# Performance work log

Hardware: AMD Instinct MI355X
Metric: run time of the kernel (lower is better)

Reference implementation:

```python
import jax, jax.numpy as jnp
import numpy as np
import math

NUM_HEADS = 8

def setup_inputs() -> dict:
    key = jax.random.key(0)
    ks = jax.random.split(key, 20)
    N, n, M, E = 4096, 3, 16, 256
    nE = 65536
    s = lambda k, shape: (jax.random.normal(k, shape, jnp.float32) * 0.02)
    return {
        "equ": jax.random.normal(ks[0], (N, n, M), jnp.float32),
        "h": jax.random.normal(ks[1], (N, E), jnp.float32),
        "edge_index": jax.random.randint(ks[2], (2, nE), 0, N),
        "edge_fea": jax.random.normal(ks[3], (nE, 4), jnp.float32),
        "W_equ": s(ks[4], (M, E)),
        "W_gproj": s(ks[5], (E, 32)),
        "W_vg": s(ks[6], (E, E)),
        "W_g1": s(ks[7], (32 * 32, 2 * E)), "b_g1": jnp.zeros((2 * E,), jnp.float32),
        "W_g2": s(ks[8], (2 * E, E)), "b_g2": jnp.zeros((E,), jnp.float32),
        "W_q": s(ks[9], (2 * E, E)), "b_q": jnp.zeros((E,), jnp.float32),
        "W_k": s(ks[10], (2 * E, E)), "b_k": jnp.zeros((E,), jnp.float32),
        "W_v": s(ks[11], (2 * E, E)), "b_v": jnp.zeros((E,), jnp.float32),
        "W_ng": s(ks[12], (E, E)), "b_ng": jnp.zeros((E,), jnp.float32),
        "W_gout": s(ks[13], (E, E)),
        "W_gdec": s(ks[14], (E, M)),
        "W_hdec": s(ks[15], (E, E)), "b_hdec": jnp.zeros((E,), jnp.float32),
    }


def reference(equ, h, edge_index, edge_fea, W_equ, W_gproj, W_vg, W_g1, b_g1,
              W_g2, b_g2, W_q, b_q, W_k, b_k, W_v, b_v, W_ng, b_ng,
              W_gout, W_gdec, W_hdec, b_hdec):
    # edge_index / edge_fea are unused in the original forward (dead args).
    N, n, M = equ.shape
    E = W_equ.shape[1]
    H = NUM_HEADS
    D = E // H
    scaling = D ** -0.5
    sqrtE = math.sqrt(E)

    g_src = (equ @ W_equ) * sqrtE                     # [N, n, E]
    h_src = h * sqrtE                                 # [N, E]

    g2 = g_src @ W_gproj                              # [N, n, 32]
    gram = jnp.einsum('nia,nib->nab', g2, g2)         # [N, 32, 32]
    g2 = gram.reshape(N, 32 * 32)
    g2 = jax.nn.relu(g2 @ W_g1 + b_g1) @ W_g2 + b_g2  # [N, E]

    h2 = jnp.concatenate([g2, h_src], axis=-1)        # [N, 2E]
    q = ((h2 @ W_q + b_q) * scaling).reshape(N, H, D)
    k = (h2 @ W_k + b_k).reshape(N, H, D)
    v = (h2 @ W_v + b_v).reshape(N, H, D)
    vg = (g_src @ W_vg).reshape(N, n, H, D)           # [N, n, H, D]

    attn = jax.nn.softmax(jnp.einsum('nhd,mhd->hnm', q, k), axis=-1)  # [H, N, N]

    out_v = jnp.einsum('hnm,mhd->nhd', attn, v).reshape(N, E)
    h_src1 = out_v @ W_ng + b_ng                      # [N, E]

    # Same attention probs reused for the vector channel (torch does repeat+bmm;
    # we broadcast instead of materializing the repeated [n*H, N, N] tensor).
    out_g = jnp.einsum('hnm,mvhd->nvhd', attn, vg).reshape(N, n, E)
    g_src1 = out_g @ W_gout                           # [N, n, E]

    g_src = g_src + g_src1
    h_src = h_src + h_src1
    equ_out = g_src @ W_gdec                          # [N, n, M]
    h_out = h_src @ W_hdec + b_hdec                   # [N, E]
    return (equ_out, h_out)
```

## Files before the change

### kernel.cpp

```cpp
#include <hip/hip_runtime.h>
#include <hip/hip_bf16.h>

typedef __attribute__((ext_vector_type(8))) short short8;
typedef __attribute__((ext_vector_type(4))) short bhalf4;
typedef __attribute__((ext_vector_type(4))) float floatx4;

constexpr int N_ = 4096;
constexpr float SQRT_E = 16.0f;
constexpr float QSCALE = 0.17677669529663687f * 1.4426950408889634f;

__device__ __forceinline__ ushort f2bf(float x) {
  __hip_bfloat16 h = __float2bfloat16(x);
  return *reinterpret_cast<ushort*>(&h);
}
__device__ __forceinline__ float bf2f(ushort b) {
  unsigned int u = ((unsigned int)b) << 16;
  return __uint_as_float(u);
}

__device__ __forceinline__ void do_transpose(
    const float* __restrict__ src, ushort* __restrict__ dsth,
    ushort* __restrict__ dstl, int R, int C, int lb, int cb_shift,
    float* smem, int hasLo)
{
  float (*tile)[33] = (float(*)[33])smem;
  const int r0 = (lb >> cb_shift) * 32;
  const int c0 = (lb & ((1 << cb_shift) - 1)) * 32;
  const int tx = threadIdx.x & 31, ty = threadIdx.x >> 5;
  #pragma unroll
  for (int p = 0; p < 4; ++p) {
    const int lr = p*8 + ty;
    tile[lr][tx] = (r0+lr < R && c0+tx < C) ? src[(size_t)(r0+lr)*C + c0 + tx] : 0.f;
  }
  __syncthreads();
  #pragma unroll
  for (int p = 0; p < 4; ++p) {
    const int dc = p*8 + ty;
    if (c0+dc < C && r0+tx < R) {
      const float v = tile[tx][dc];
      const ushort hi = f2bf(v);
      dsth[(size_t)(c0+dc)*R + r0 + tx] = hi;
      if (hasLo) dstl[(size_t)(c0+dc)*R + r0 + tx] = f2bf(v - bf2f(hi));
    }
  }
}

__global__ __launch_bounds__(256) void k_prep(
    const float* __restrict__ equ, const float* __restrict__ h,
    const float* __restrict__ W_equ, const float* __restrict__ W_gproj,
    const float* __restrict__ W_g1, const float* __restrict__ W_g2,
    const float* __restrict__ W_q, const float* __restrict__ W_k,
    const float* __restrict__ W_v, const float* __restrict__ W_vg,
    const float* __restrict__ W_ng, const float* __restrict__ W_gout,
    const float* __restrict__ W_hdec, const float* __restrict__ W_gdec,
    ushort* __restrict__ Wg1t, ushort* __restrict__ Wg2t,
    ushort* __restrict__ Wth, ushort* __restrict__ Wtl,
    ushort* __restrict__ Wvgt, ushort* __restrict__ Wngt,
    ushort* __restrict__ Wgoutt, ushort* __restrict__ Whdect,
    ushort* __restrict__ Wgdect,
    ushort* __restrict__ h2h, ushort* __restrict__ h2l,
    ushort* __restrict__ g_src_b, ushort* __restrict__ gram_b,
    float* __restrict__ pre0)
{
  __shared__ __align__(16) float smem[1120];
  const int b = blockIdx.x;
  const int t = threadIdx.x;

  if (b < 512) {
    do_transpose(W_g1, Wg1t, nullptr, 1024, 512, b, 4, smem, 0);
  } else if (b < 640) {
    do_transpose(W_g2, Wg2t, nullptr, 512, 256, b-512, 3, smem, 0);
  } else if (b < 768) {
    do_transpose(W_q, Wth, Wtl, 512, 256, b-640, 3, smem, 1);
  } else if (b < 896) {
    do_transpose(W_k, Wth + 256*512, Wtl + 256*512, 512, 256, b-768, 3, smem, 1);
  } else if (b < 1024) {
    do_transpose(W_v, Wth + 512*512, Wtl + 512*512, 512, 256, b-896, 3, smem, 1);
  } else if (b < 1088) {
    do_transpose(W_vg, Wvgt, nullptr, 256, 256, b-1024, 3, smem, 0);
  } else if (b < 1152) {
    do_transpose(W_ng, Wngt, nullptr, 256, 256, b-1088, 3, smem, 0);
  } else if (b < 1216) {
    do_transpose(W_gout, Wgoutt, nullptr, 256, 256, b-1152, 3, smem, 0);
  } else if (b < 1280) {
    do_transpose(W_hdec, Whdect, nullptr, 256, 256, b-1216, 3, smem, 0);
  } else if (b < 1288) {
    do_transpose(W_gdec, Wgdect, nullptr, 256, 16, b-1280, 0, smem, 0);
  } else if (b < 5384) {
    const int i = b - 1288;
    const float v = h[(size_t)i*256 + t] * SQRT_E;
    const ushort hi = f2bf(v);
    h2h[(size_t)i*512 + 256 + t] = hi;
    h2l[(size_t)i*512 + 256 + t] = f2bf(v - bf2f(hi));
  } else {
    float* eq   = smem;
    float* gs   = smem + 48;
    float* g2p  = smem + 816;
    float* part = smem + 912;
    const int i = b - 5384;
    if (t < 48) eq[t] = equ[(size_t)i*48 + t];
    __syncthreads();
    #pragma unroll
    for (int j = 0; j < 3; ++j) {
      float s = 0.f;
      #pragma unroll
      for (int m = 0; m < 16; ++m) s += eq[j*16+m] * W_equ[m*256 + t];
      s *= SQRT_E;
      gs[j*256 + t] = s;
      g_src_b[((size_t)i*3 + j)*256 + t] = f2bf(s);
    }
    __syncthreads();
    if (t < 192) {
      const int o = t % 96, half = t / 96;
      const int j = o >> 5, a = o & 31;
      const int e0 = half * 128;
      float s = 0.f;
      for (int e = 0; e < 128; ++e)
        s += gs[j*256 + e0 + e] * W_gproj[(size_t)(e0+e)*32 + a];
      part[t] = s;
    }
    __syncthreads();
    if (t < 96) g2p[t] = part[t] + part[96 + t];
    __syncthreads();
    #pragma unroll
    for (int r = 0; r < 4; ++r) {
      const int idx = r*256 + t;
      const int a = idx >> 5, bb = idx & 31;
      const float s = g2p[a]*g2p[bb] + g2p[32+a]*g2p[32+bb] + g2p[64+a]*g2p[64+bb];
      gram_b[(size_t)i*1024 + idx] = f2bf(s);
    }
    if (t < 192) {
      const int j = t >> 6, ks = (t >> 4) & 3, mc = t & 15;
      const int e0 = ks * 64;
      float s = 0.f;
      for (int e = 0; e < 64; ++e)
        s += gs[j*256 + e0 + e] * W_gdec[(size_t)(e0 + e)*16 + mc];
      part[t] = s;
    }
    __syncthreads();
    if (t < 48) {
      const int j = t >> 4, mc = t & 15;
      pre0[((size_t)i*3 + j)*16 + mc] =
          part[j*64 + mc] + part[j*64 + 16 + mc] +
          part[j*64 + 32 + mc] + part[j*64 + 48 + mc];
    }
  }
}

template<int KTOT>
__device__ __forceinline__ void gemm_core(
    const ushort* __restrict__ A, const ushort* __restrict__ Bt,
    int bM, int bN, floatx4 acc[4], ushort* As, ushort* Bs)
{
  const int t = threadIdx.x;
  const int wave = t >> 6, lane = t & 63, quad = lane >> 4, m = lane & 15;
  #pragma unroll
  for (int ct = 0; ct < 4; ++ct) acc[ct] = {0.f, 0.f, 0.f, 0.f};
  const int ca = t*2, cb = t*2 + 1;
  const int ra = ca >> 3, pa = ca & 7;
  const int rb = cb >> 3, pb = cb & 7;
  const ushort* pA0 = A  + (size_t)(bM+ra)*KTOT + pa*8;
  const ushort* pA1 = A  + (size_t)(bM+rb)*KTOT + pb*8;
  const ushort* pB0 = Bt + (size_t)(bN+ra)*KTOT + pa*8;
  const ushort* pB1 = Bt + (size_t)(bN+rb)*KTOT + pb*8;
  short8 rA0 = *(const short8*)pA0, rA1 = *(const short8*)pA1;
  short8 rB0 = *(const short8*)pB0, rB1 = *(const short8*)pB1;
  for (int k0 = 0; k0 < KTOT; k0 += 64) {
    __syncthreads();
    *(short8*)&As[ra*72 + pa*8] = rA0;
    *(short8*)&As[rb*72 + pb*8] = rA1;
    *(short8*)&Bs[ra*72 + pa*8] = rB0;
    *(short8*)&Bs[rb*72 + pb*8] = rB1;
    if (k0 + 64 < KTOT) {
      pA0 += 64; pA1 += 64; pB0 += 64; pB1 += 64;
      rA0 = *(const short8*)pA0; rA1 = *(const short8*)pA1;
      rB0 = *(const short8*)pB0; rB1 = *(const short8*)pB1;
    }
    __syncthreads();
    #pragma unroll
    for (int ks = 0; ks < 2; ++ks) {
      const short8 af = *(const short8*)&As[(wave*16 + m)*72 + ks*32 + quad*8];
      #pragma unroll
      for (int ct = 0; ct < 4; ++ct) {
        const short8 bf = *(const short8*)&Bs[(ct*16 + m)*72 + ks*32 + quad*8];
        acc[ct] = __builtin_amdgcn_mfma_f32_16x16x32_bf16(af, bf, acc[ct], 0, 0, 0);
      }
    }
  }
}

template<int KTOT>
__device__ __forceinline__ void gemm_core3(
    const ushort* __restrict__ Ah, const ushort* __restrict__ Al,
    const ushort* __restrict__ Bth, const ushort* __restrict__ Btl,
    int bM, int bN, floatx4 acc[4],
    ushort* Ash, ushort* Asl, ushort* Bsh, ushort* Bsl)
{
  const int t = threadIdx.x;
  const int wave = t >> 6, lane = t & 63, quad = lane >> 4, m = lane & 15;
  #pragma unroll
  for (int ct = 0; ct < 4; ++ct) acc[ct] = {0.f, 0.f, 0.f, 0.f};
  const int ca = t*2, cb = t*2 + 1;
  const int ra = ca >> 3, pa = ca & 7;
  const int rb = cb >> 3, pb = cb & 7;
  const ushort* pAh0 = Ah  + (size_t)(bM+ra)*KTOT + pa*8;
  const ushort* pAh1 = Ah  + (size_t)(bM+rb)*KTOT + pb*8;
  const ushort* pAl0 = Al  + (size_t)(bM+ra)*KTOT + pa*8;
  const ushort* pAl1 = Al  + (size_t)(bM+rb)*KTOT + pb*8;
  const ushort* pBh0 = Bth + (size_t)(bN+ra)*KTOT + pa*8;
  const ushort* pBh1 = Bth + (size_t)(bN+rb)*KTOT + pb*8;
  const ushort* pBl0 = Btl + (size_t)(bN+ra)*KTOT + pa*8;
  const ushort* pBl1 = Btl + (size_t)(bN+rb)*KTOT + pb*8;
  short8 rAh0 = *(const short8*)pAh0, rAh1 = *(const short8*)pAh1;
  short8 rAl0 = *(const short8*)pAl0, rAl1 = *(const short8*)pAl1;
  short8 rBh0 = *(const short8*)pBh0, rBh1 = *(const short8*)pBh1;
  short8 rBl0 = *(const short8*)pBl0, rBl1 = *(const short8*)pBl1;
  for (int k0 = 0; k0 < KTOT; k0 += 64) {
    __syncthreads();
    *(short8*)&Ash[ra*72 + pa*8] = rAh0;
    *(short8*)&Ash[rb*72 + pb*8] = rAh1;
    *(short8*)&Asl[ra*72 + pa*8] = rAl0;
    *(short8*)&Asl[rb*72 + pb*8] = rAl1;
    *(short8*)&Bsh[ra*72 + pa*8] = rBh0;
    *(short8*)&Bsh[rb*72 + pb*8] = rBh1;
    *(short8*)&Bsl[ra*72 + pa*8] = rBl0;
    *(short8*)&Bsl[rb*72 + pb*8] = rBl1;
    if (k0 + 64 < KTOT) {
      pAh0 += 64; pAh1 += 64; pAl0 += 64; pAl1 += 64;
      pBh0 += 64; pBh1 += 64; pBl0 += 64; pBl1 += 64;
      rAh0 = *(const short8*)pAh0; rAh1 = *(const short8*)pAh1;
      rAl0 = *(const short8*)pAl0; rAl1 = *(const short8*)pAl1;
      rBh0 = *(const short8*)pBh0; rBh1 = *(const short8*)pBh1;
      rBl0 = *(const short8*)pBl0; rBl1 = *(const short8*)pBl1;
    }
    __syncthreads();
    #pragma unroll
    for (int ks = 0; ks < 2; ++ks) {
      const short8 ah = *(const short8*)&Ash[(wave*16 + m)*72 + ks*32 + quad*8];
      const short8 al = *(const short8*)&Asl[(wave*16 + m)*72 + ks*32 + quad*8];
      #pragma unroll
      for (int ct = 0; ct < 4; ++ct) {
        const short8 bh = *(const short8*)&Bsh[(ct*16 + m)*72 + ks*32 + quad*8];
        const short8 bl = *(const short8*)&Bsl[(ct*16 + m)*72 + ks*32 + quad*8];
        acc[ct] = __builtin_amdgcn_mfma_f32_16x16x32_bf16(ah, bl, acc[ct], 0, 0, 0);
        acc[ct] = __builtin_amdgcn_mfma_f32_16x16x32_bf16(al, bh, acc[ct], 0, 0, 0);
        acc[ct] = __builtin_amdgcn_mfma_f32_16x16x32_bf16(ah, bh, acc[ct], 0, 0, 0);
      }
    }
  }
}

__global__ __launch_bounds__(256) void k_g1(
    const ushort* __restrict__ gram_b, const ushort* __restrict__ Wg1t,
    const float* __restrict__ b_g1, ushort* __restrict__ hidden)
{
  __shared__ __align__(16) ushort As[64*72], Bs[64*72];
  floatx4 acc[4];
  const int bM = blockIdx.x*64, bN = blockIdx.y*64;
  gemm_core<1024>(gram_b, Wg1t, bM, bN, acc, As, Bs);
  const int lane = threadIdx.x & 63, wave = threadIdx.x >> 6;
  const int quad = lane >> 4, m = lane & 15;
  #pragma unroll
  for (int ct = 0; ct < 4; ++ct) {
    const int c = bN + ct*16 + m;
    #pragma unroll
    for (int r = 0; r < 4; ++r) {
      const int i = bM + wave*16 + quad*4 + r;
      hidden[(size_t)i*512 + c] = f2bf(fmaxf(acc[ct][r] + b_g1[c], 0.f));
    }
  }
}

__global__ __launch_bounds__(256) void k_g2(
    const ushort* __restrict__ hidden, const ushort* __restrict__ Wg2t,
    const float* __restrict__ b_g2, ushort* __restrict__ h2h, ushort* __restrict__ h2l)
{
  __shared__ __align__(16) ushort As[64*72], Bs[64*72];
  floatx4 acc[4];
  const int bM = blockIdx.x*64, bN = blockIdx.y*64;
  gemm_core<512>(hidden, Wg2t, bM, bN, acc, As, Bs);
  const int lane = threadIdx.x & 63, wave = threadIdx.x >> 6;
  const int quad = lane >> 4, m = lane & 15;
  #pragma unroll
  for (int ct = 0; ct < 4; ++ct) {
    const int c = bN + ct*16 + m;
    #pragma unroll
    for (int r = 0; r < 4; ++r) {
      const int i = bM + wave*16 + quad*4 + r;
      const float s = acc[ct][r] + b_g2[c];
      const ushort hi = f2bf(s);
      h2h[(size_t)i*512 + c] = hi;
      h2l[(size_t)i*512 + c] = f2bf(s - bf2f(hi));
    }
  }
}

__global__ __launch_bounds__(256) void k_g34(
    const ushort* __restrict__ h2h, const ushort* __restrict__ h2l,
    const ushort* __restrict__ Wth, const ushort* __restrict__ Wtl,
    const float* __restrict__ b_q, const float* __restrict__ b_k,
    const float* __restrict__ b_v,
    const ushort* __restrict__ g_src_b, const ushort* __restrict__ Wvgt,
    float* __restrict__ q_ws, ushort* __restrict__ kh,
    ushort* __restrict__ vt)
{
  __shared__ __align__(16) ushort S0[64*72], S1[64*72], S2[64*72], S3[64*72];
  const int lb = blockIdx.y*192 + blockIdx.x;
  const int lane = threadIdx.x & 63, wave = threadIdx.x >> 6;
  const int quad = lane >> 4, m = lane & 15;
  floatx4 acc[4];
  if (lb < 768) {
    const int bM = (lb & 63)*64, bN = (lb >> 6)*64;
    if (bN < 512) {
      gemm_core3<512>(h2h, h2l, Wth, Wtl, bM, bN, acc, S0, S1, S2, S3);
      #pragma unroll
      for (int ct = 0; ct < 4; ++ct) {
        const int c = bN + ct*16 + m;
        #pragma unroll
        for (int r = 0; r < 4; ++r) {
          const int i = bM + wave*16 + quad*4 + r;
          if (c < 256) {
            const float s = acc[ct][r] + b_q[c];
            q_ws[((size_t)(c >> 5)*N_ + i)*32 + (c & 31)] = s * QSCALE;
          } else {
            const int cc = c - 256;
            const float s = acc[ct][r] + b_k[cc];
            kh[((size_t)(cc >> 5)*N_ + i)*32 + (cc & 31)] = f2bf(s);
          }
        }
      }
    } else {
      gemm_core<512>(h2h, Wth, bM, bN, acc, S0, S1);
      #pragma unroll
      for (int ct = 0; ct < 4; ++ct) {
        const int cc = bN + ct*16 + m - 512;
        #pragma unroll
        for (int r = 0; r < 4; ++r) {
          const int i = bM + wave*16 + quad*4 + r;
          const float s = acc[ct][r] + b_v[cc];
          vt[((size_t)(cc >> 5)*128 + (cc & 31))*N_ + i] = f2bf(s);
        }
      }
    }
  } else {
    const int lb2 = lb - 768;
    const int bM = (lb2 >> 2)*64, bN = (lb2 & 3)*64;
    gemm_core<256>(g_src_b, Wvgt, bM, bN, acc, S0, S1);
    #pragma unroll
    for (int ct = 0; ct < 4; ++ct) {
      const int c = bN + ct*16 + m;
      const int hh = c >> 5, d = c & 31;
      #pragma unroll
      for (int r = 0; r < 4; ++r) {
        const int i3 = bM + wave*16 + quad*4 + r;
        const int i = i3 / 3, j = i3 - 3*i;
        vt[((size_t)hh*128 + 32 + j*32 + d)*N_ + i] = f2bf(acc[ct][r]);
      }
    }
  }
}

__global__ __launch_bounds__(256, 8) void k3_attn(
    const float* __restrict__ q_ws, const ushort* __restrict__ kh,
    const ushort* __restrict__ vt,
    ushort* __restrict__ Po0, ushort* __restrict__ Po1,
    ushort* __restrict__ Po2, ushort* __restrict__ Po3,
    float* __restrict__ Pml)
{
  __shared__ __align__(16) ushort Khs[64*40];
  __shared__ __align__(16) ushort Vs[128*64];

  const int t    = threadIdx.x;
  const int wave = t >> 6;
  const int lane = t & 63;
  const int quad = lane >> 4;
  const int m    = lane & 15;
  const int h    = blockIdx.y;
  const int s    = blockIdx.z;
  const int n0q  = blockIdx.x * 64;

  const int ktb = s * 16;
  const int kte = ktb + 16;

  union { short8 v; ushort u[8]; } Aqh, Aql;
  {
    const float* qp = q_ws + ((size_t)h*N_ + n0q + wave*16 + m)*32 + quad*8;
    #pragma unroll
    for (int jj = 0; jj < 8; ++jj) {
      const float x = qp[jj];
      const ushort hi = f2bf(x);
      Aqh.u[jj] = hi;
      Aql.u[jj] = f2bf(x - bf2f(hi));
    }
  }

  union { short8 v; ushort u[8]; } onesf;
  {
    const ushort ov = (m == 0) ? (ushort)0x3F80 : (ushort)0;
    #pragma unroll
    for (int jj = 0; jj < 8; ++jj) onesf.u[jj] = ov;
  }

  floatx4 Of[8];
  #pragma unroll
  for (int nt = 0; nt < 8; ++nt) Of[nt] = {0.f, 0.f, 0.f, 0.f};
  floatx4 Of8 = {0.f, 0.f, 0.f, 0.f};
  float mi = -3.0e38f;

  const int krow = t >> 2, kch = (t & 3) * 8;
  const ushort* pKh = kh + ((size_t)h*N_ + ktb*64 + krow)*32 + kch;

  const ushort* pV[4];
  int wv0[4], wv1[4];
  #pragma unroll
  for (int p = 0; p < 4; ++p) {
    const int idx = p*256 + t, row = idx >> 3, g = idx & 7;
    pV[p] = vt + ((size_t)h*128 + row)*N_ + ktb*64 + g*8;
    const int sb0  = 32*(g>>2) + 16*(g&1) + 4*((g>>1)&1);
    const int blk0 = sb0 >> 3, off = sb0 & 4, r7 = row & 7;
    wv0[p] = row*64 + ((blk0       ^ r7) * 8) + off;
    wv1[p] = row*64 + (((blk0 + 1) ^ r7) * 8) + off;
  }

  short8 rK0 = *(const short8*)pKh;
  short8 rV[4];
  #pragma unroll
  for (int p = 0; p < 4; ++p) rV[p] = *(const short8*)pV[p];

  const int x7 = m & 7;

  for (int kt = ktb; kt < kte; ++kt) {
    __syncthreads();
    *(short8*)&Khs[krow*40 + kch] = rK0;
    #pragma unroll
    for (int p = 0; p < 4; ++p) {
      union { short8 v; bhalf4 h2[2]; } tmp;
      tmp.v = rV[p];
      *(bhalf4*)&Vs[wv0[p]] = tmp.h2[0];
      *(bhalf4*)&Vs[wv1[p]] = tmp.h2[1];
    }
    if (kt + 1 < kte) {
      pKh += 2048;
      rK0 = *(const short8*)pKh;
      #pragma unroll
      for (int p = 0; p < 4; ++p) { pV[p] += 64; rV[p] = *(const short8*)pV[p]; }
    }
    __syncthreads();

    floatx4 sf[4];
    #pragma unroll
    for (int kb = 0; kb < 4; ++kb) {
      const short8 bkh = *(const short8*)&Khs[(kb*16 + m)*40 + quad*8];
      floatx4 sv = {0.f, 0.f, 0.f, 0.f};
      sv = __builtin_amdgcn_mfma_f32_16x16x32_bf16(bkh, Aql.v, sv, 0, 0, 0);
      sv = __builtin_amdgcn_mfma_f32_16x16x32_bf16(bkh, Aqh.v, sv, 0, 0, 0);
      sf[kb] = sv;
    }

    float nm = fmaxf(fmaxf(sf[0][0], sf[0][1]), fmaxf(sf[0][2], sf[0][3]));
    nm = fmaxf(nm, fmaxf(fmaxf(sf[1][0], sf[1][1]), fmaxf(sf[1][2], sf[1][3])));
    nm = fmaxf(nm, fmaxf(fmaxf(sf[2][0], sf[2][1]), fmaxf(sf[2][2], sf[2][3])));
    nm = fmaxf(nm, fmaxf(fmaxf(sf[3][0], sf[3][1]), fmaxf(sf[3][2], sf[3][3])));
    nm = fmaxf(nm, __shfl_xor(nm, 16));
    nm = fmaxf(nm, __shfl_xor(nm, 32));

    if (__any(nm > mi + 20.f)) {
      const float mn = fmaxf(mi, nm);
      const float al = exp2f(mi - mn);
      mi = mn;
      #pragma unroll
      for (int nt = 0; nt < 8; ++nt) {
        Of[nt][0] *= al; Of[nt][1] *= al; Of[nt][2] *= al; Of[nt][3] *= al;
      }
      Of8[0] *= al; Of8[1] *= al; Of8[2] *= al; Of8[3] *= al;
    }

    const float base = 1064866805.0f - mi*8388608.0f;
    union { short8 v; unsigned int u[4]; } pk[2];
    #pragma unroll
    for (int kb = 0; kb < 4; ++kb) {
      int p0 = (int)(sf[kb][0]*8388608.0f + base); p0 = p0 < 0 ? 0 : p0;
      int p1 = (int)(sf[kb][1]*8388608.0f + base); p1 = p1 < 0 ? 0 : p1;
      int p2 = (int)(sf[kb][2]*8388608.0f + base); p2 = p2 < 0 ? 0 : p2;
      int p3 = (int)(sf[kb][3]*8388608.0f + base); p3 = p3 < 0 ? 0 : p3;
      pk[kb >> 1].u[(kb & 1)*2 + 0] = ((unsigned)p0 >> 16) | ((unsigned)p1 & 0xffff0000u);
      pk[kb >> 1].u[(kb & 1)*2 + 1] = ((unsigned)p2 >> 16) | ((unsigned)p3 & 0xffff0000u);
    }

    #pragma unroll
    for (int ks = 0; ks < 2; ++ks) {
      #pragma unroll
      for (int nt = 0; nt < 8; ++nt) {
        const short8 av = *(const short8*)&Vs[(nt*16 + m)*64 + (((ks*4 + quad) ^ x7) * 8)];
        Of[nt] = __builtin_amdgcn_mfma_f32_16x16x32_bf16(av, pk[ks].v, Of[nt], 0, 0, 0);
      }
      Of8 = __builtin_amdgcn_mfma_f32_16x16x32_bf16(onesf.v, pk[ks].v, Of8, 0, 0, 0);
    }
  }

  const float denom = __shfl(Of8[0], m);
  const float linv = 1.0f / denom;

  ushort* Po = (s == 0) ? Po0 : ((s == 1) ? Po1 : ((s == 2) ? Po2 : Po3));
  const int n = n0q + wave*16 + m;
  #pragma unroll
  for (int nt = 0; nt < 8; ++nt) {
    unsigned int lo = (unsigned)f2bf(Of[nt][0] * linv) | ((unsigned)f2bf(Of[nt][1] * linv) << 16);
    unsigned int hi = (unsigned)f2bf(Of[nt][2] * linv) | ((unsigned)f2bf(Of[nt][3] * linv) << 16);
    uint2 pkd; pkd.x = lo; pkd.y = hi;
    *(uint2*)&Po[((size_t)h*N_ + n)*128 + nt*16 + quad*4] = pkd;
  }
  if (quad == 0) {
    Pml[(((size_t)s*8 + h)*N_ + n)*2 + 0] = mi;
    Pml[(((size_t)s*8 + h)*N_ + n)*2 + 1] = Of8[0];
  }
}

__global__ __launch_bounds__(256) void k_merge(
    const ushort* __restrict__ Po0, const ushort* __restrict__ Po1,
    const ushort* __restrict__ Po2, const ushort* __restrict__ Po3,
    const float* __restrict__ Pml,
    ushort* __restrict__ out_v_b, ushort* __restrict__ out_g_b)
{
  const int idx = blockIdx.x*256 + threadIdx.x;
  const int c0 = (idx & 15) * 8;
  const int n  = (idx >> 4) & 4095;
  const int h  = idx >> 16;
  float mm[4], ll[4];
  #pragma unroll
  for (int s = 0; s < 4; ++s) {
    mm[s] = Pml[(((size_t)s*8 + h)*N_ + n)*2 + 0];
    ll[s] = Pml[(((size_t)s*8 + h)*N_ + n)*2 + 1];
  }
  const float M = fmaxf(fmaxf(mm[0], mm[1]), fmaxf(mm[2], mm[3]));
  float w[4], tot = 0.f;
  #pragma unroll
  for (int s = 0; s < 4; ++s) { w[s] = exp2f(mm[s] - M) * ll[s]; tot += w[s]; }
  const float inv = 1.0f / tot;
  union { short8 v; ushort u[8]; } a, b, c, d, res;
  a.v = *(const short8*)&Po0[((size_t)h*N_ + n)*128 + c0];
  b.v = *(const short8*)&Po1[((size_t)h*N_ + n)*128 + c0];
  c.v = *(const short8*)&Po2[((size_t)h*N_ + n)*128 + c0];
  d.v = *(const short8*)&Po3[((size_t)h*N_ + n)*128 + c0];
  #pragma unroll
  for (int j = 0; j < 8; ++j)
    res.u[j] = f2bf((w[0]*bf2f(a.u[j]) + w[1]*bf2f(b.u[j]) +
                     w[2]*bf2f(c.u[j]) + w[3]*bf2f(d.u[j])) * inv);
  if (c0 < 32) {
    *(short8*)&out_v_b[(size_t)n*256 + h*32 + c0] = res.v;
  } else {
    const int j = (c0 - 32) >> 5, cc = (c0 - 32) & 31;
    *(short8*)&out_g_b[((size_t)n*3 + j)*256 + h*32 + cc] = res.v;
  }
}

__global__ __launch_bounds__(256) void k56ab(
    const ushort* __restrict__ out_v_b, const ushort* __restrict__ Wngt,
    const float* __restrict__ b_ng, const float* __restrict__ h,
    ushort* __restrict__ tmp_b,
    const ushort* __restrict__ out_g_b, const ushort* __restrict__ Wgoutt,
    ushort* __restrict__ gsum_b)
{
  __shared__ __align__(16) ushort As[64*72], Bs[64*72];
  floatx4 acc[4];
  const int lane = threadIdx.x & 63, wave = threadIdx.x >> 6;
  const int quad = lane >> 4, m = lane & 15;
  const int bN = blockIdx.y*64;
  if (blockIdx.x < 64) {
    const int bM = blockIdx.x*64;
    gemm_core<256>(out_v_b, Wngt, bM, bN, acc, As, Bs);
    #pragma unroll
    for (int ct = 0; ct < 4; ++ct) {
      const int c = bN + ct*16 + m;
      #pragma unroll
      for (int r = 0; r < 4; ++r) {
        const int i = bM + wave*16 + quad*4 + r;
        tmp_b[(size_t)i*256 + c] =
            f2bf(acc[ct][r] + b_ng[c] + h[(size_t)i*256 + c] * SQRT_E);
      }
    }
  } else {
    const int bM = (blockIdx.x - 64)*64;
    gemm_core<256>(out_g_b, Wgoutt, bM, bN, acc, As, Bs);
    #pragma unroll
    for (int ct = 0; ct < 4; ++ct) {
      const int c = bN + ct*16 + m;
      #pragma unroll
      for (int r = 0; r < 4; ++r) {
        const int i = bM + wave*16 + quad*4 + r;
        gsum_b[(size_t)i*256 + c] = f2bf(acc[ct][r]);
      }
    }
  }
}

__global__ __launch_bounds__(256) void k56cd(
    const ushort* __restrict__ tmp_b, const ushort* __restrict__ Whdect,
    const float* __restrict__ b_hdec,
    const ushort* __restrict__ gsum_b, const ushort* __restrict__ Wgdect,
    const float* __restrict__ pre0,
    float* __restrict__ out)
{
  __shared__ __align__(16) ushort As[64*72], Bs[64*72];
  const int t = threadIdx.x;
  const int lane = t & 63, wave = t >> 6;
  const int quad = lane >> 4, m = lane & 15;
  if (blockIdx.x < 64) {
    floatx4 acc[4];
    const int bM = blockIdx.x*64, bN = blockIdx.y*64;
    gemm_core<256>(tmp_b, Whdect, bM, bN, acc, As, Bs);
    #pragma unroll
    for (int ct = 0; ct < 4; ++ct) {
      const int c = bN + ct*16 + m;
      #pragma unroll
      for (int r = 0; r < 4; ++r) {
        const int i = bM + wave*16 + quad*4 + r;
        out[196608 + (size_t)i*256 + c] = acc[ct][r] + b_hdec[c];
      }
    }
  } else if (blockIdx.y == 0) {
    const int bM = (blockIdx.x - 64)*64;
    floatx4 acc = {0.f, 0.f, 0.f, 0.f};
    const int row = t >> 2, kq = (t & 3) * 8;
    for (int k0 = 0; k0 < 256; k0 += 32) {
      __syncthreads();
      *(short8*)&As[row*40 + kq] = *(const short8*)&gsum_b[(size_t)(bM+row)*256 + k0 + kq];
      if (t < 64)
        *(short8*)&Bs[(t>>2)*40 + kq] = *(const short8*)&Wgdect[(size_t)(t>>2)*256 + k0 + kq];
      __syncthreads();
      const short8 af = *(const short8*)&As[(wave*16 + m)*40 + quad*8];
      const short8 bf = *(const short8*)&Bs[m*40 + quad*8];
      acc = __builtin_amdgcn_mfma_f32_16x16x32_bf16(af, bf, acc, 0, 0, 0);
    }
    #pragma unroll
    for (int r = 0; r < 4; ++r) {
      const int i3 = bM + wave*16 + quad*4 + r;
      out[(size_t)i3*16 + m] = acc[r] + pre0[(size_t)i3*16 + m];
    }
  }
}

extern "C" void kernel_launch(void* const* d_in, const int* in_sizes, int n_in,
                              void* d_out, int out_size, void* d_ws, size_t ws_size,
                              hipStream_t stream) {
  const float* equ    = (const float*)d_in[0];
  const float* h      = (const float*)d_in[1];
  const float* W_equ  = (const float*)d_in[4];
  const float* W_gproj= (const float*)d_in[5];
  const float* W_vg   = (const float*)d_in[6];
  const float* W_g1   = (const float*)d_in[7];
  const float* b_g1   = (const float*)d_in[8];
  const float* W_g2   = (const float*)d_in[9];
  const float* b_g2   = (const float*)d_in[10];
  const float* W_q    = (const float*)d_in[11];
  const float* b_q    = (const float*)d_in[12];
  const float* W_k    = (const float*)d_in[13];
  const float* b_k    = (const float*)d_in[14];
  const float* W_v    = (const float*)d_in[15];
  const float* b_v    = (const float*)d_in[16];
  const float* W_ng   = (const float*)d_in[17];
  const float* b_ng   = (const float*)d_in[18];
  const float* W_gout = (const float*)d_in[19];
  const float* W_gdec = (const float*)d_in[20];
  const float* W_hdec = (const float*)d_in[21];
  const float* b_hdec = (const float*)d_in[22];
  float* out = (float*)d_out;

  char* wsb = (char*)d_ws;
  constexpr size_t MiB = 1048576;
  float*  q_ws    = (float*) (wsb +  0*MiB);
  ushort* kh      = (ushort*)(wsb +  4*MiB);
  float*  Pml     = (float*) (wsb +  6*MiB);
  float*  pre0    = (float*) (wsb +  7*MiB);
  ushort* vt      = (ushort*)(wsb +  8*MiB);
  ushort* h2h     = (ushort*)(wsb + 17*MiB);
  ushort* h2l     = (ushort*)(wsb + 21*MiB);
  ushort* g_src_b = (ushort*)(wsb + 25*MiB);
  ushort* wbase   = (ushort*)(wsb + 31*MiB);
  ushort* Wg1t = wbase;
  ushort* Wg2t = wbase + 524288;
  ushort* Wth  = wbase + 655360;
  ushort* Wtl  = wbase + 1048576;
  ushort* Wvgt = wbase + 1441792;
  ushort* gram_b  = (ushort*)(wsb + 34*MiB);
  ushort* hidden  = (ushort*)(wsb + 42*MiB);
  ushort* Po0     = (ushort*)(wsb + 17*MiB);
  ushort* Po1     = (ushort*)(wsb + 25*MiB);
  ushort* Po2     = (ushort*)(wsb + 34*MiB);
  ushort* Po3     = (ushort*)(wsb + 42*MiB);
  ushort* wbase2  = (ushort*)(wsb + 50*MiB);
  ushort* Wngt   = wbase2;
  ushort* Wgoutt = wbase2 + 65536;
  ushort* Whdect = wbase2 + 131072;
  ushort* Wgdect = wbase2 + 196608;
  ushort* out_v_b = (ushort*)(wsb +  4*MiB);
  ushort* out_g_b = (ushort*)(wsb +  8*MiB);
  ushort* tmp_b   = (ushort*)(wsb + 17*MiB);
  ushort* gsum_b  = (ushort*)(wsb + 25*MiB);

  k_prep<<<9480, 256, 0, stream>>>(
      equ, h, W_equ, W_gproj, W_g1, W_g2, W_q, W_k, W_v,
      W_vg, W_ng, W_gout, W_hdec, W_gdec,
      Wg1t, Wg2t, Wth, Wtl, Wvgt, Wngt, Wgoutt, Whdect, Wgdect,
      h2h, h2l, g_src_b, gram_b, pre0);

  k_g1<<<dim3(64, 8), 256, 0, stream>>>(gram_b, Wg1t, b_g1, hidden);
  k_g2<<<dim3(64, 4), 256, 0, stream>>>(hidden, Wg2t, b_g2, h2h, h2l);
  k_g34<<<dim3(192, 8), 256, 0, stream>>>(h2h, h2l, Wth, Wtl, b_q, b_k, b_v,
                                          g_src_b, Wvgt, q_ws, kh, vt);

  dim3 g3(64, 8, 4);
  k3_attn<<<g3, 256, 0, stream>>>(q_ws, kh, vt, Po0, Po1, Po2, Po3, Pml);
  k_merge<<<2048, 256, 0, stream>>>(Po0, Po1, Po2, Po3, Pml, out_v_b, out_g_b);

  k56ab<<<dim3(256, 4), 256, 0, stream>>>(out_v_b, Wngt, b_ng, h, tmp_b,
                                          out_g_b, Wgoutt, gsum_b);
  k56cd<<<dim3(256, 4), 256, 0, stream>>>(tmp_b, Whdect, b_hdec,
                                          gsum_b, Wgdect, pre0, out);
}
```

Measured before the change: 279.9 us.

## Process two query tiles per wave in attention kernel to reuse K/V LDS tiles

Each wave of the split-K attention kernel now handles two 16-row query groups, so a block covers 128 queries and the grid is halved. Every K and V tile staged in LDS, and each V fragment read from LDS, feeds twice as many MFMAs, which halves global K/V traffic and LDS reads per query. The denominator is now passed through a small shared buffer instead of a shuffle. The cost is about twice the accumulator registers, with launch bounds lowered to 3 blocks, so occupancy drops and there are fewer blocks to hide latency.

```diff
diff --git a/kernel.cpp b/kernel.cpp
--- a/kernel.cpp
+++ b/kernel.cpp
@@ -360,7 +360,7 @@
   }
 }
 
-__global__ __launch_bounds__(256, 8) void k3_attn(
+__global__ __launch_bounds__(256, 3) void k3_attn(
     const float* __restrict__ q_ws, const ushort* __restrict__ kh,
     const ushort* __restrict__ vt,
     ushort* __restrict__ Po0, ushort* __restrict__ Po1,
@@ -369,6 +369,7 @@
 {
   __shared__ __align__(16) ushort Khs[64*40];
   __shared__ __align__(16) ushort Vs[128*64];
+  __shared__ float li_s[128];
 
   const int t    = threadIdx.x;
   const int wave = t >> 6;
@@ -377,20 +378,21 @@
   const int m    = lane & 15;
   const int h    = blockIdx.y;
   const int s    = blockIdx.z;
-  const int n0q  = blockIdx.x * 64;
+  const int n0q  = blockIdx.x * 128;
 
   const int ktb = s * 16;
   const int kte = ktb + 16;
 
-  union { short8 v; ushort u[8]; } Aqh, Aql;
-  {
-    const float* qp = q_ws + ((size_t)h*N_ + n0q + wave*16 + m)*32 + quad*8;
+  union { short8 v; ushort u[8]; } Aqh[2], Aql[2];
+  #pragma unroll
+  for (int g = 0; g < 2; ++g) {
+    const float* qp = q_ws + ((size_t)h*N_ + n0q + (wave*2+g)*16 + m)*32 + quad*8;
     #pragma unroll
     for (int jj = 0; jj < 8; ++jj) {
       const float x = qp[jj];
       const ushort hi = f2bf(x);
-      Aqh.u[jj] = hi;
-      Aql.u[jj] = f2bf(x - bf2f(hi));
+      Aqh[g].u[jj] = hi;
+      Aql[g].u[jj] = f2bf(x - bf2f(hi));
     }
   }
 
@@ -401,11 +403,15 @@
     for (int jj = 0; jj < 8; ++jj) onesf.u[jj] = ov;
   }
 
-  floatx4 Of[8];
-  #pragma unroll
-  for (int nt = 0; nt < 8; ++nt) Of[nt] = {0.f, 0.f, 0.f, 0.f};
-  floatx4 Of8 = {0.f, 0.f, 0.f, 0.f};
-  float mi = -3.0e38f;
+  floatx4 Of[2][8];
+  #pragma unroll
+  for (int g = 0; g < 2; ++g)
+    #pragma unroll
+    for (int nt = 0; nt < 8; ++nt) Of[g][nt] = {0.f, 0.f, 0.f, 0.f};
+  floatx4 Of8[2];
+  Of8[0] = {0.f, 0.f, 0.f, 0.f};
+  Of8[1] = {0.f, 0.f, 0.f, 0.f};
+  float mi[2] = {-3.0e38f, -3.0e38f};
 
   const int krow = t >> 2, kch = (t & 3) * 8;
   const ushort* pKh = kh + ((size_t)h*N_ + ktb*64 + krow)*32 + kch;
@@ -447,72 +453,89 @@
     }
     __syncthreads();
 
-    floatx4 sf[4];
-    #pragma unroll
-    for (int kb = 0; kb < 4; ++kb) {
-      const short8 bkh = *(const short8*)&Khs[(kb*16 + m)*40 + quad*8];
-      floatx4 sv = {0.f, 0.f, 0.f, 0.f};
-      sv = __builtin_amdgcn_mfma_f32_16x16x32_bf16(bkh, Aql.v, sv, 0, 0, 0);
-      sv = __builtin_amdgcn_mfma_f32_16x16x32_bf16(bkh, Aqh.v, sv, 0, 0, 0);
-      sf[kb] = sv;
-    }
-
-    float nm = fmaxf(fmaxf(sf[0][0], sf[0][1]), fmaxf(sf[0][2], sf[0][3]));
-    nm = fmaxf(nm, fmaxf(fmaxf(sf[1][0], sf[1][1]), fmaxf(sf[1][2], sf[1][3])));
-    nm = fmaxf(nm, fmaxf(fmaxf(sf[2][0], sf[2][1]), fmaxf(sf[2][2], sf[2][3])));
-    nm = fmaxf(nm, fmaxf(fmaxf(sf[3][0], sf[3][1]), fmaxf(sf[3][2], sf[3][3])));
-    nm = fmaxf(nm, __shfl_xor(nm, 16));
-    nm = fmaxf(nm, __shfl_xor(nm, 32));
-
-    if (__any(nm > mi + 20.f)) {
-      const float mn = fmaxf(mi, nm);
-      const float al = exp2f(mi - mn);
-      mi = mn;
-      #pragma unroll
-      for (int nt = 0; nt < 8; ++nt) {
-        Of[nt][0] *= al; Of[nt][1] *= al; Of[nt][2] *= al; Of[nt][3] *= al;
-      }
-      Of8[0] *= al; Of8[1] *= al; Of8[2] *= al; Of8[3] *= al;
-    }
-
-    const float base = 1064866805.0f - mi*8388608.0f;
-    union { short8 v; unsigned int u[4]; } pk[2];
-    #pragma unroll
-    for (int kb = 0; kb < 4; ++kb) {
-      int p0 = (int)(sf[kb][0]*8388608.0f + base); p0 = p0 < 0 ? 0 : p0;
-      int p1 = (int)(sf[kb][1]*8388608.0f + base); p1 = p1 < 0 ? 0 : p1;
-      int p2 = (int)(sf[kb][2]*8388608.0f + base); p2 = p2 < 0 ? 0 : p2;
-      int p3 = (int)(sf[kb][3]*8388608.0f + base); p3 = p3 < 0 ? 0 : p3;
-      pk[kb >> 1].u[(kb & 1)*2 + 0] = ((unsigned)p0 >> 16) | ((unsigned)p1 & 0xffff0000u);
-      pk[kb >> 1].u[(kb & 1)*2 + 1] = ((unsigned)p2 >> 16) | ((unsigned)p3 & 0xffff0000u);
-    }
-
-    #pragma unroll
-    for (int ks = 0; ks < 2; ++ks) {
-      #pragma unroll
-      for (int nt = 0; nt < 8; ++nt) {
-        const short8 av = *(const short8*)&Vs[(nt*16 + m)*64 + (((ks*4 + quad) ^ x7) * 8)];
-        Of[nt] = __builtin_amdgcn_mfma_f32_16x16x32_bf16(av, pk[ks].v, Of[nt], 0, 0, 0);
-      }
-      Of8 = __builtin_amdgcn_mfma_f32_16x16x32_bf16(onesf.v, pk[ks].v, Of8, 0, 0, 0);
-    }
-  }
-
-  const float denom = __shfl(Of8[0], m);
-  const float linv = 1.0f / denom;
+    union { short8 v; unsigned int u[4]; } pkA[2], pkB[2];
+    #pragma unroll
+    for (int g = 0; g < 2; ++g) {
+      floatx4 sf[4];
+      #pragma unroll
+      for (int kb = 0; kb < 4; ++kb) {
+        const short8 bkh = *(const short8*)&Khs[(kb*16 + m)*40 + quad*8];
+        floatx4 sv = {0.f, 0.f, 0.f, 0.f};
+        sv = __builtin_amdgcn_mfma_f32_16x16x32_bf16(bkh, Aql[g].v, sv, 0, 0, 0);
+        sv = __builtin_amdgcn_mfma_f32_16x16x32_bf16(bkh, Aqh[g].v, sv, 0, 0, 0);
+        sf[kb] = sv;
+      }
+
+      float nm = fmaxf(fmaxf(sf[0][0], sf[0][1]), fmaxf(sf[0][2], sf[0][3]));
+      nm = fmaxf(nm, fmaxf(fmaxf(sf[1][0], sf[1][1]), fmaxf(sf[1][2], sf[1][3])));
+      nm = fmaxf(nm, fmaxf(fmaxf(sf[2][0], sf[2][1]), fmaxf(sf[2][2], sf[2][3])));
+      nm = fmaxf(nm, fmaxf(fmaxf(sf[3][0], sf[3][1]), fmaxf(sf[3][2], sf[3][3])));
+      nm = fmaxf(nm, __shfl_xor(nm, 16));
+      nm = fmaxf(nm, __shfl_xor(nm, 32));
+
+      if (__any(nm > mi[g] + 20.f)) {
+        const float mn = fmaxf(mi[g], nm);
+        const float al = exp2f(mi[g] - mn);
+        mi[g] = mn;
+        #pragma unroll
+        for (int nt = 0; nt < 8; ++nt) {
+          Of[g][nt][0] *= al; Of[g][nt][1] *= al;
+          Of[g][nt][2] *= al; Of[g][nt][3] *= al;
+        }
+        Of8[g][0] *= al; Of8[g][1] *= al; Of8[g][2] *= al; Of8[g][3] *= al;
+      }
+
+      const float base = 1064866805.0f - mi[g]*8388608.0f;
+      #pragma unroll
+      for (int kb = 0; kb < 4; ++kb) {
+        int p0 = (int)(sf[kb][0]*8388608.0f + base); p0 = p0 < 0 ? 0 : p0;
+        int p1 = (int)(sf[kb][1]*8388608.0f + base); p1 = p1 < 0 ? 0 : p1;
+        int p2 = (int)(sf[kb][2]*8388608.0f + base); p2 = p2 < 0 ? 0 : p2;
+        int p3 = (int)(sf[kb][3]*8388608.0f + base); p3 = p3 < 0 ? 0 : p3;
+        const unsigned wlo = ((unsigned)p0 >> 16) | ((unsigned)p1 & 0xffff0000u);
+        const unsigned whi = ((unsigned)p2 >> 16) | ((unsigned)p3 & 0xffff0000u);
+        if (kb < 2) { pkA[g].u[kb*2] = wlo; pkA[g].u[kb*2+1] = whi; }
+        else        { pkB[g].u[(kb-2)*2] = wlo; pkB[g].u[(kb-2)*2+1] = whi; }
+      }
+    }
+
+    #pragma unroll
+    for (int nt = 0; nt < 8; ++nt) {
+      const short8 av0 = *(const short8*)&Vs[(nt*16 + m)*64 + ((quad ^ x7) * 8)];
+      Of[0][nt] = __builtin_amdgcn_mfma_f32_16x16x32_bf16(av0, pkA[0].v, Of[0][nt], 0, 0, 0);
+      Of[1][nt] = __builtin_amdgcn_mfma_f32_16x16x32_bf16(av0, pkA[1].v, Of[1][nt], 0, 0, 0);
+      const short8 av1 = *(const short8*)&Vs[(nt*16 + m)*64 + (((4 + quad) ^ x7) * 8)];
+      Of[0][nt] = __builtin_amdgcn_mfma_f32_16x16x32_bf16(av1, pkB[0].v, Of[0][nt], 0, 0, 0);
+      Of[1][nt] = __builtin_amdgcn_mfma_f32_16x16x32_bf16(av1, pkB[1].v, Of[1][nt], 0, 0, 0);
+    }
+    Of8[0] = __builtin_amdgcn_mfma_f32_16x16x32_bf16(onesf.v, pkA[0].v, Of8[0], 0, 0, 0);
+    Of8[1] = __builtin_amdgcn_mfma_f32_16x16x32_bf16(onesf.v, pkA[1].v, Of8[1], 0, 0, 0);
+    Of8[0] = __builtin_amdgcn_mfma_f32_16x16x32_bf16(onesf.v, pkB[0].v, Of8[0], 0, 0, 0);
+    Of8[1] = __builtin_amdgcn_mfma_f32_16x16x32_bf16(onesf.v, pkB[1].v, Of8[1], 0, 0, 0);
+  }
+
+  if (quad == 0) {
+    li_s[wave*32 + m]      = Of8[0][0];
+    li_s[wave*32 + 16 + m] = Of8[1][0];
+  }
+  __syncthreads();
 
   ushort* Po = (s == 0) ? Po0 : ((s == 1) ? Po1 : ((s == 2) ? Po2 : Po3));
-  const int n = n0q + wave*16 + m;
-  #pragma unroll
-  for (int nt = 0; nt < 8; ++nt) {
-    unsigned int lo = (unsigned)f2bf(Of[nt][0] * linv) | ((unsigned)f2bf(Of[nt][1] * linv) << 16);
-    unsigned int hi = (unsigned)f2bf(Of[nt][2] * linv) | ((unsigned)f2bf(Of[nt][3] * linv) << 16);
-    uint2 pkd; pkd.x = lo; pkd.y = hi;
-    *(uint2*)&Po[((size_t)h*N_ + n)*128 + nt*16 + quad*4] = pkd;
-  }
-  if (quad == 0) {
-    Pml[(((size_t)s*8 + h)*N_ + n)*2 + 0] = mi;
-    Pml[(((size_t)s*8 + h)*N_ + n)*2 + 1] = Of8[0];
+  #pragma unroll
+  for (int g = 0; g < 2; ++g) {
+    const float linv = 1.0f / li_s[wave*32 + g*16 + m];
+    const int n = n0q + (wave*2 + g)*16 + m;
+    #pragma unroll
+    for (int nt = 0; nt < 8; ++nt) {
+      unsigned int lo = (unsigned)f2bf(Of[g][nt][0] * linv) | ((unsigned)f2bf(Of[g][nt][1] * linv) << 16);
+      unsigned int hi = (unsigned)f2bf(Of[g][nt][2] * linv) | ((unsigned)f2bf(Of[g][nt][3] * linv) << 16);
+      uint2 pkd; pkd.x = lo; pkd.y = hi;
+      *(uint2*)&Po[((size_t)h*N_ + n)*128 + nt*16 + quad*4] = pkd;
+    }
+    if (quad == 0) {
+      Pml[(((size_t)s*8 + h)*N_ + n)*2 + 0] = mi[g];
+      Pml[(((size_t)s*8 + h)*N_ + n)*2 + 1] = Of8[g][0];
+    }
   }
 }
 
@@ -709,7 +732,7 @@
   k_g34<<<dim3(192, 8), 256, 0, stream>>>(h2h, h2l, Wth, Wtl, b_q, b_k, b_v,
                                           g_src_b, Wvgt, q_ws, kh, vt);
 
-  dim3 g3(64, 8, 4);
+  dim3 g3(32, 8, 4);
   k3_attn<<<g3, 256, 0, stream>>>(q_ws, kh, vt, Po0, Po1, Po2, Po3, Pml);
   k_merge<<<2048, 256, 0, stream>>>(Po0, Po1, Po2, Po3, Pml, out_v_b, out_g_b);
 
```

New measurement: 297.0 us. 1.06x slower.
